# Kernel optimization log

Measured on AMD Instinct MI355X. Metric: run time of the kernel, lower is better.

Reference implementation:

```python
import jax, jax.numpy as jnp
import numpy as np

D_MODEL = 1024
N_HEAD = 16
D_HEAD = D_MODEL // N_HEAD
NEG = -1e9


def setup_inputs() -> dict:
    key = jax.random.key(0)
    ks = jax.random.split(key, 11)
    B, T, C = 4, 2048, D_MODEL
    s = 1.0 / np.sqrt(C)
    return {
        "q": jax.random.normal(ks[0], (B, T, C), jnp.float32),
        "k": jax.random.normal(ks[1], (B, T, C), jnp.float32),
        "v": jax.random.normal(ks[2], (B, T, C), jnp.float32),
        "w_q": jax.random.normal(ks[3], (C, C), jnp.float32) * s,
        "b_q": jnp.zeros((C,), jnp.float32),
        "w_k": jax.random.normal(ks[4], (C, C), jnp.float32) * s,
        "b_k": jnp.zeros((C,), jnp.float32),
        "w_v": jax.random.normal(ks[5], (C, C), jnp.float32) * s,
        "b_v": jnp.zeros((C,), jnp.float32),
        "w_o": jax.random.normal(ks[6], (C, C), jnp.float32) * s,
        "b_o": jnp.zeros((C,), jnp.float32),
    }


def reference(q, k, v, w_q, b_q, w_k, b_k, w_v, b_v, w_o, b_o):
    B, T, C = q.shape
    # projections; weights stored as [in, out]
    qh = (q @ w_q + b_q).reshape(B, T, N_HEAD, D_HEAD).transpose(0, 2, 1, 3)
    kh = (k @ w_k + b_k).reshape(B, T, N_HEAD, D_HEAD).transpose(0, 2, 1, 3)
    vh = (v @ w_v + b_v).reshape(B, T, N_HEAD, D_HEAD).transpose(0, 2, 1, 3)
    scores = jnp.einsum("bhqd,bhkd->bhqk", qh, kh) / jnp.sqrt(
        jnp.asarray(D_HEAD, qh.dtype))
    causal = jnp.tril(jnp.ones((T, T), dtype=bool))  # [T,T]
    scores = jnp.where(causal[None, None], scores, NEG)
    attn = jax.nn.softmax(scores, axis=-1)
    out = jnp.einsum("bhqk,bhkd->bhqd", attn, vh)
    out = out.transpose(0, 2, 1, 3).reshape(B, T, C)
    return out @ w_o + b_o
```

## Files before the change

### kernel.cpp

```cpp
#include <hip/hip_runtime.h>
#include <hip/hip_bf16.h>
#include <cstdint>
#include <cstddef>

#define DEVI static __device__ __forceinline__

typedef __attribute__((ext_vector_type(8))) short short8;
typedef __attribute__((ext_vector_type(4))) float f32x4;

typedef __attribute__((address_space(1))) const unsigned int as1c_uint;
typedef __attribute__((address_space(3))) unsigned int as3_uint;

constexpr int Bn = 4, Tn = 2048, Cn = 1024, Hn = 16, Dn = 64;
constexpr int Mtot = Bn * Tn;
#define QSCALE (0.125f * 1.44269504088896340736f)

DEVI unsigned short f2bf(float f) {
  unsigned u = __float_as_uint(f);
  u += 0x7fffu + ((u >> 16) & 1u);
  return (unsigned short)(u >> 16);
}
DEVI unsigned short f2bf_t(float f) {
  return (unsigned short)(__float_as_uint(f) >> 16);
}

DEVI void async16(const void* g, void* l) {
  __builtin_amdgcn_global_load_lds((as1c_uint*)g, (as3_uint*)l, 16, 0, 0);
}

__global__ __launch_bounds__(256) void transpose_cvt4(
    const float* __restrict__ w0, const float* __restrict__ w1,
    const float* __restrict__ w2, const float* __restrict__ w3,
    unsigned short* __restrict__ o0, unsigned short* __restrict__ o1,
    unsigned short* __restrict__ o2, unsigned short* __restrict__ o3) {
  __shared__ float tile[32][33];
  const int z = blockIdx.z;
  const float* w = z == 0 ? w0 : z == 1 ? w1 : z == 2 ? w2 : w3;
  unsigned short* wT = z == 0 ? o0 : z == 1 ? o1 : z == 2 ? o2 : o3;
  int n0 = blockIdx.x * 32, k0 = blockIdx.y * 32;
  int tx = threadIdx.x, ty = threadIdx.y;
#pragma unroll
  for (int r = 0; r < 32; r += 8)
    tile[ty + r][tx] = w[(size_t)(k0 + ty + r) * Cn + n0 + tx];
  __syncthreads();
  const int t = ty * 32 + tx;
  const int n_l = t >> 3;
  const int kq = (t & 7) * 4;
  const int n = n0 + n_l, k = k0 + kq;
  ushort4 pk;
#pragma unroll
  for (int e = 0; e < 4; ++e) ((unsigned short*)&pk)[e] = f2bf(tile[kq + e][n_l]);
  size_t idx = (size_t)((((n >> 4) * 32 + (k >> 5)) * 64 + ((k >> 3) & 3) * 16 + (n & 15))) * 8 + (k & 7);
  *(ushort4*)&wT[idx] = pk;
}

DEVI short8 xfrag(const unsigned short* Xlds, int i, int kc, int l15, int l4) {
  int row = i * 16 + l15;
  return *(const short8*)&Xlds[row * 1024 + (((kc * 4 + l4) ^ (row & 7)) * 8)];
}

template <int IB, int NJ, bool SWAP>
DEVI void proj_core(const unsigned short* __restrict__ wF,
                    const unsigned short* Xlds, int njb, int lane,
                    f32x4 (&acc)[IB][NJ]) {
  const int l15 = lane & 15, l4 = lane >> 4;
  const short8* wp = (const short8*)wF;
  short8 wfA[NJ], wfB[NJ];
#pragma unroll
  for (int j = 0; j < NJ; ++j) wfA[j] = wp[(size_t)((njb + j) * 32) * 64 + lane];
#pragma unroll 1
  for (int kc = 0; kc < 32; kc += 2) {
#pragma unroll
    for (int j = 0; j < NJ; ++j)
      wfB[j] = wp[(size_t)((njb + j) * 32 + kc + 1) * 64 + lane];
    short8 xf[IB];
#pragma unroll
    for (int i = 0; i < IB; ++i) xf[i] = xfrag(Xlds, i, kc, l15, l4);
#pragma unroll
    for (int i = 0; i < IB; ++i)
#pragma unroll
      for (int j = 0; j < NJ; ++j)
        acc[i][j] = SWAP
            ? __builtin_amdgcn_mfma_f32_16x16x32_bf16(xf[i], wfA[j], acc[i][j], 0, 0, 0)
            : __builtin_amdgcn_mfma_f32_16x16x32_bf16(wfA[j], xf[i], acc[i][j], 0, 0, 0);
    if (kc + 2 < 32) {
#pragma unroll
      for (int j = 0; j < NJ; ++j)
        wfA[j] = wp[(size_t)((njb + j) * 32 + kc + 2) * 64 + lane];
    }
#pragma unroll
    for (int i = 0; i < IB; ++i) xf[i] = xfrag(Xlds, i, kc + 1, l15, l4);
#pragma unroll
    for (int i = 0; i < IB; ++i)
#pragma unroll
      for (int j = 0; j < NJ; ++j)
        acc[i][j] = SWAP
            ? __builtin_amdgcn_mfma_f32_16x16x32_bf16(xf[i], wfB[j], acc[i][j], 0, 0, 0)
            : __builtin_amdgcn_mfma_f32_16x16x32_bf16(wfB[j], xf[i], acc[i][j], 0, 0, 0);
  }
}

DEVI void stage64_f32(const float* __restrict__ src, int m0,
                      unsigned short* Xlds, int tid) {
#pragma unroll
  for (int it = 0; it < 8; ++it) {
    int g = it * 1024 + tid;
    int row = g >> 7, slot = g & 127;
    const float4* p = (const float4*)(src + (size_t)(m0 + row) * Cn + slot * 8);
    float4 a = p[0], b = p[1];
    short8 sv;
    sv[0] = (short)f2bf(a.x); sv[1] = (short)f2bf(a.y);
    sv[2] = (short)f2bf(a.z); sv[3] = (short)f2bf(a.w);
    sv[4] = (short)f2bf(b.x); sv[5] = (short)f2bf(b.y);
    sv[6] = (short)f2bf(b.z); sv[7] = (short)f2bf(b.w);
    *(short8*)&Xlds[row * 1024 + ((slot ^ (row & 7)) * 8)] = sv;
  }
}

DEVI void stage64_bf(const unsigned short* __restrict__ src, int m0,
                     unsigned short* Xlds, int tid) {
#pragma unroll
  for (int it = 0; it < 8; ++it) {
    int s = it * 1024 + tid;
    int row = s >> 7, sl = s & 127;
    async16(src + (size_t)(m0 + row) * Cn + ((sl ^ (row & 7)) * 8),
            Xlds + (size_t)(it * 1024 + (tid & ~63)) * 8);
  }
}

__global__ __launch_bounds__(1024, 4) void proj_qkv(
    const float* __restrict__ xqf, const float* __restrict__ xkf,
    const float* __restrict__ xvf, const unsigned short* __restrict__ wFq,
    const unsigned short* __restrict__ wFk, const unsigned short* __restrict__ wFv,
    const float* __restrict__ bq, const float* __restrict__ bk,
    const float* __restrict__ bv, unsigned short* __restrict__ oq,
    unsigned short* __restrict__ ok, unsigned short* __restrict__ ov) {
  __shared__ unsigned short Xlds[64 * 1024];
  const int tid = threadIdx.x, lane = tid & 63, w = tid >> 6;
  const int l15 = lane & 15, l4 = lane >> 4;
  const int bid = blockIdx.x;
  const int z = bid >> 8;
  const int r = bid & 255;
  const int m0 = (r >> 1) * 64;
  const int nh = r & 1;
  const float* xz = z == 0 ? xqf : z == 1 ? xkf : xvf;
  const unsigned short* wF = z == 0 ? wFq : z == 1 ? wFk : wFv;
  const float* bias = z == 0 ? bq : z == 1 ? bk : bv;

  stage64_f32(xz, m0, Xlds, tid);
  __syncthreads();

  const f32x4 zf = {0.f, 0.f, 0.f, 0.f};
  f32x4 acc[4][2];
#pragma unroll
  for (int i = 0; i < 4; ++i)
#pragma unroll
    for (int j = 0; j < 2; ++j) acc[i][j] = zf;

  const int njb = nh * 32 + w * 2;
  if (z < 2)
    proj_core<4, 2, false>(wF, Xlds, njb, lane, acc);
  else
    proj_core<4, 2, true>(wF, Xlds, njb, lane, acc);

  const int b = m0 >> 11, t0loc = m0 & 2047;
  if (z < 2) {
    unsigned short* o = z == 0 ? oq : ok;
    const float scale = z == 0 ? QSCALE : 1.f;
#pragma unroll
    for (int j = 0; j < 2; ++j) {
      int ng = njb + j;
      int h = ng >> 2, d0 = (ng & 3) * 16 + l4 * 4;
      float4 bv4 = *(const float4*)&bias[ng * 16 + l4 * 4];
#pragma unroll
      for (int i = 0; i < 4; ++i) {
        int t = t0loc + i * 16 + l15;
        ushort4 pk;
        pk.x = f2bf((acc[i][j][0] + bv4.x) * scale);
        pk.y = f2bf((acc[i][j][1] + bv4.y) * scale);
        pk.z = f2bf((acc[i][j][2] + bv4.z) * scale);
        pk.w = f2bf((acc[i][j][3] + bv4.w) * scale);
        *(ushort4*)&o[((size_t)((b * Hn + h) * Tn + t)) * Dn + d0] = pk;
      }
    }
  } else {
#pragma unroll
    for (int j = 0; j < 2; ++j) {
      int n = (njb + j) * 16 + l15;
      int h = n >> 6, d = n & 63;
      float bvl = bias[n];
#pragma unroll
      for (int i = 0; i < 4; ++i) {
        int t0 = t0loc + i * 16 + l4 * 4;
        ushort4 pk;
        pk.x = f2bf(acc[i][j][0] + bvl);
        pk.y = f2bf(acc[i][j][1] + bvl);
        pk.z = f2bf(acc[i][j][2] + bvl);
        pk.w = f2bf(acc[i][j][3] + bvl);
        *(ushort4*)&ov[((size_t)((b * Hn + h) * Dn + d)) * Tn + t0] = pk;
      }
    }
  }
}

__global__ __launch_bounds__(1024, 4) void proj_out(
    const unsigned short* __restrict__ A, const unsigned short* __restrict__ wFo,
    const float* __restrict__ bias, float* __restrict__ o) {
  __shared__ unsigned short Xlds[64 * 1024];
  const int tid = threadIdx.x, lane = tid & 63, w = tid >> 6;
  const int l15 = lane & 15, l4 = lane >> 4;
  const int bid = blockIdx.x;
  const int m0 = (bid >> 1) * 64, nh = bid & 1;

  stage64_bf(A, m0, Xlds, tid);
  __syncthreads();

  const f32x4 zf = {0.f, 0.f, 0.f, 0.f};
  f32x4 acc[4][2];
#pragma unroll
  for (int i = 0; i < 4; ++i)
#pragma unroll
    for (int j = 0; j < 2; ++j) acc[i][j] = zf;

  const int njb = nh * 32 + w * 2;
  proj_core<4, 2, false>(wFo, Xlds, njb, lane, acc);

#pragma unroll
  for (int j = 0; j < 2; ++j) {
    int ng = njb + j;
    float4 bv4 = *(const float4*)&bias[ng * 16 + l4 * 4];
#pragma unroll
    for (int i = 0; i < 4; ++i) {
      int m = m0 + i * 16 + l15;
      float4 ov4;
      ov4.x = acc[i][j][0] + bv4.x;
      ov4.y = acc[i][j][1] + bv4.y;
      ov4.z = acc[i][j][2] + bv4.z;
      ov4.w = acc[i][j][3] + bv4.w;
      *(float4*)&o[(size_t)m * Cn + ng * 16 + l4 * 4] = ov4;
    }
  }
}

__global__ __launch_bounds__(512) void attn_kernel(const unsigned short* __restrict__ qh,
                                                   const unsigned short* __restrict__ kh,
                                                   const unsigned short* __restrict__ vt,
                                                   unsigned short* __restrict__ obf) {
  __shared__ unsigned short Ks[2][64 * 64];
  __shared__ unsigned short Vs[2][64 * 64];
  __shared__ unsigned short Ps[8][16 * 72];

  const int tid = threadIdx.x, lane = tid & 63, w = tid >> 6;
  const int l15 = lane & 15, l4 = lane >> 4;
  const int swz = l15 & 7;

  const int bid = blockIdx.x;
  const int j = bid >> 3;
  const int bh = (bid & 7) * 8 + (j & 7);
  const int pair = j >> 3;
  const unsigned short* qb = qh + (size_t)bh * Tn * Dn;
  const unsigned short* kb = kh + (size_t)bh * Tn * Dn;
  const unsigned short* vb = vt + (size_t)bh * Dn * Tn;
  const int b = bh >> 4, h = bh & 15;

  const int srow = lane >> 3, sslot = (lane & 7) ^ (lane >> 3);

  const f32x4 z = {0.f, 0.f, 0.f, 0.f};
  const short ob = (short)0x3F80;
  const short8 ones = {ob, ob, ob, ob, ob, ob, ob, ob};

#pragma unroll 1
  for (int half = 0; half < 2; ++half) {
    const int qt = half == 0 ? pair : 15 - pair;
    const int q0 = qt * 128;
    const int qrow = q0 + w * 16 + l15;

    short8 qf0 = *(const short8*)(qb + (size_t)qrow * Dn + l4 * 8);
    short8 qf1 = *(const short8*)(qb + (size_t)qrow * Dn + 32 + l4 * 8);

    f32x4 o[4];
#pragma unroll
    for (int nd = 0; nd < 4; ++nd) o[nd] = z;
    f32x4 osum = z;

    const int nt = (q0 >> 6) + 2;
    const int ntw = ((q0 + w * 16 + 15) >> 6) + 1;

    {
      const unsigned short* ksrc = kb + (size_t)(w * 8 + srow) * Dn + sslot * 8;
      const unsigned short* vsrc = vb + (size_t)(w * 8 + srow) * Tn + sslot * 8;
      async16(ksrc, &Ks[0][w * 512]);
      async16(vsrc, &Vs[0][w * 512]);
    }

#pragma unroll 1
    for (int t = 0; t < nt; ++t) {
      const int cur = t & 1;
      if (t + 1 < nt) {
        const int kv1 = (t + 1) * 64;
        const unsigned short* ksrc = kb + (size_t)(kv1 + w * 8 + srow) * Dn + sslot * 8;
        const unsigned short* vsrc = vb + (size_t)(w * 8 + srow) * Tn + kv1 + sslot * 8;
        async16(ksrc, &Ks[cur ^ 1][w * 512]);
        async16(vsrc, &Vs[cur ^ 1][w * 512]);
        asm volatile("s_waitcnt vmcnt(2)" ::: "memory");
      } else {
        asm volatile("s_waitcnt vmcnt(0)" ::: "memory");
      }
      __builtin_amdgcn_s_barrier();
      __builtin_amdgcn_sched_barrier(0);

      if (t < ntw) {
        const unsigned short* Kc = &Ks[cur][0];
        const unsigned short* Vc = &Vs[cur][0];

        f32x4 s[4];
#pragma unroll
        for (int ni = 0; ni < 4; ++ni) s[ni] = z;
        __builtin_amdgcn_s_setprio(1);
#pragma unroll
        for (int ni = 0; ni < 4; ++ni) {
          const int rb = (ni * 16 + l15) * 64;
          short8 kf0 = *(const short8*)&Kc[rb + ((l4 ^ swz) * 8)];
          short8 kf1 = *(const short8*)&Kc[rb + (((4 + l4) ^ swz) * 8)];
          s[ni] = __builtin_amdgcn_mfma_f32_16x16x32_bf16(kf0, qf0, s[ni], 0, 0, 0);
          s[ni] = __builtin_amdgcn_mfma_f32_16x16x32_bf16(kf1, qf1, s[ni], 0, 0, 0);
        }
        __builtin_amdgcn_s_setprio(0);

        short8 vf[8];
#pragma unroll
        for (int nd = 0; nd < 4; ++nd) {
          const int rb = (nd * 16 + l15) * 64;
          vf[nd * 2]     = *(const short8*)&Vc[rb + ((l4 ^ swz) * 8)];
          vf[nd * 2 + 1] = *(const short8*)&Vc[rb + (((4 + l4) ^ swz) * 8)];
        }

        const int kq = qrow - t * 64;
        const bool edge = (t * 64 + 63 > q0 + w * 16);
        if (!edge) {
#pragma unroll
          for (int ni = 0; ni < 4; ++ni) {
            ushort4 pk;
#pragma unroll
            for (int r = 0; r < 4; ++r)
              ((unsigned short*)&pk)[r] = f2bf_t(__builtin_amdgcn_exp2f(s[ni][r]));
            *(ushort4*)&Ps[w][l15 * 72 + ni * 16 + l4 * 4] = pk;
          }
        } else {
#pragma unroll
          for (int ni = 0; ni < 4; ++ni) {
            ushort4 pk;
#pragma unroll
            for (int r = 0; r < 4; ++r) {
              float e = __builtin_amdgcn_exp2f(s[ni][r]);
              if ((ni * 16 + l4 * 4 + r) > kq) e = 0.f;
              ((unsigned short*)&pk)[r] = f2bf_t(e);
            }
            *(ushort4*)&Ps[w][l15 * 72 + ni * 16 + l4 * 4] = pk;
          }
        }
        asm volatile("s_waitcnt lgkmcnt(0)" ::: "memory");
        __builtin_amdgcn_sched_barrier(0);

        short8 pf0 = *(const short8*)&Ps[w][l15 * 72 + l4 * 8];
        short8 pf1 = *(const short8*)&Ps[w][l15 * 72 + 32 + l4 * 8];
        __builtin_amdgcn_s_setprio(1);
        osum = __builtin_amdgcn_mfma_f32_16x16x32_bf16(pf0, ones, osum, 0, 0, 0);
        osum = __builtin_amdgcn_mfma_f32_16x16x32_bf16(pf1, ones, osum, 0, 0, 0);
#pragma unroll
        for (int nd = 0; nd < 4; ++nd) {
          o[nd] = __builtin_amdgcn_mfma_f32_16x16x32_bf16(pf0, vf[nd * 2], o[nd], 0, 0, 0);
          o[nd] = __builtin_amdgcn_mfma_f32_16x16x32_bf16(pf1, vf[nd * 2 + 1], o[nd], 0, 0, 0);
        }
        __builtin_amdgcn_s_setprio(0);
      }

      __builtin_amdgcn_sched_barrier(0);
      __builtin_amdgcn_s_barrier();
    }

#pragma unroll
    for (int r = 0; r < 4; ++r) {
      float inv = __builtin_amdgcn_rcpf(osum[r]);
      int tq = q0 + w * 16 + l4 * 4 + r;
      size_t base = ((size_t)(b * Tn + tq)) * Cn + h * 64;
#pragma unroll
      for (int nd = 0; nd < 4; ++nd)
        obf[base + nd * 16 + l15] = f2bf(o[nd][r] * inv);
    }
  }
}

extern "C" void kernel_launch(void* const* d_in, const int* in_sizes, int n_in,
                              void* d_out, int out_size, void* d_ws, size_t ws_size,
                              hipStream_t stream) {
  const float* q   = (const float*)d_in[0];
  const float* k   = (const float*)d_in[1];
  const float* v   = (const float*)d_in[2];
  const float* w_q = (const float*)d_in[3];
  const float* b_q = (const float*)d_in[4];
  const float* w_k = (const float*)d_in[5];
  const float* b_k = (const float*)d_in[6];
  const float* w_v = (const float*)d_in[7];
  const float* b_v = (const float*)d_in[8];
  const float* w_o = (const float*)d_in[9];
  const float* b_o = (const float*)d_in[10];

  char* ws = (char*)d_ws;
  const size_t MB = 1u << 20;
  unsigned short* qhp  = (unsigned short*)(ws);
  unsigned short* khp  = (unsigned short*)(ws + 16 * MB);
  unsigned short* vtp  = (unsigned short*)(ws + 32 * MB);
  unsigned short* aout = (unsigned short*)(ws + 48 * MB);
  unsigned short* wqT  = (unsigned short*)(ws + 64 * MB);
  unsigned short* wkT  = (unsigned short*)(ws + 66 * MB);
  unsigned short* wvT  = (unsigned short*)(ws + 68 * MB);
  unsigned short* woT  = (unsigned short*)(ws + 70 * MB);

  transpose_cvt4<<<dim3(32, 32, 4), dim3(32, 8), 0, stream>>>(
      w_q, w_k, w_v, w_o, wqT, wkT, wvT, woT);

  proj_qkv<<<768, 1024, 0, stream>>>(q, k, v, wqT, wkT, wvT,
                                     b_q, b_k, b_v, qhp, khp, vtp);

  attn_kernel<<<512, 512, 0, stream>>>(qhp, khp, vtp, aout);

  proj_out<<<256, 1024, 0, stream>>>(aout, woT, b_o, (float*)d_out);
}
```

Before: 169.1 us.

## Process q/k/v projections in one persistent block with prefetched input staging

The QKV projection kernel now launches 256 blocks that each loop over the three projections, instead of 768 blocks that each handle one. The next input tile's fp32 global loads are issued into registers before the current MFMA loop runs, so load latency overlaps compute. The cost is 64 extra VGPRs per thread for the staging buffer, with the launch-bounds occupancy hint dropped. There are also only 256 blocks for 256 CUs, one block per CU, which cuts the parallelism available to hide latency.

```diff
diff --git a/kernel.cpp b/kernel.cpp
--- a/kernel.cpp
+++ b/kernel.cpp
@@ -100,14 +100,24 @@
   }
 }
 
-DEVI void stage64_f32(const float* __restrict__ src, int m0,
-                      unsigned short* Xlds, int tid) {
+DEVI void stage_issue(const float* __restrict__ src, int m0, int tid,
+                      float4 (&st)[16]) {
 #pragma unroll
   for (int it = 0; it < 8; ++it) {
     int g = it * 1024 + tid;
     int row = g >> 7, slot = g & 127;
     const float4* p = (const float4*)(src + (size_t)(m0 + row) * Cn + slot * 8);
-    float4 a = p[0], b = p[1];
+    st[it * 2] = p[0];
+    st[it * 2 + 1] = p[1];
+  }
+}
+
+DEVI void stage_write(const float4 (&st)[16], unsigned short* Xlds, int tid) {
+#pragma unroll
+  for (int it = 0; it < 8; ++it) {
+    int g = it * 1024 + tid;
+    int row = g >> 7, slot = g & 127;
+    float4 a = st[it * 2], b = st[it * 2 + 1];
     short8 sv;
     sv[0] = (short)f2bf(a.x); sv[1] = (short)f2bf(a.y);
     sv[2] = (short)f2bf(a.z); sv[3] = (short)f2bf(a.w);
@@ -128,7 +138,7 @@
   }
 }
 
-__global__ __launch_bounds__(1024, 4) void proj_qkv(
+__global__ __launch_bounds__(1024) void proj_qkv(
     const float* __restrict__ xqf, const float* __restrict__ xkf,
     const float* __restrict__ xvf, const unsigned short* __restrict__ wFq,
     const unsigned short* __restrict__ wFk, const unsigned short* __restrict__ wFv,
@@ -139,65 +149,78 @@
   const int tid = threadIdx.x, lane = tid & 63, w = tid >> 6;
   const int l15 = lane & 15, l4 = lane >> 4;
   const int bid = blockIdx.x;
-  const int z = bid >> 8;
-  const int r = bid & 255;
-  const int m0 = (r >> 1) * 64;
-  const int nh = r & 1;
-  const float* xz = z == 0 ? xqf : z == 1 ? xkf : xvf;
-  const unsigned short* wF = z == 0 ? wFq : z == 1 ? wFk : wFv;
-  const float* bias = z == 0 ? bq : z == 1 ? bk : bv;
-
-  stage64_f32(xz, m0, Xlds, tid);
-  __syncthreads();
-
-  const f32x4 zf = {0.f, 0.f, 0.f, 0.f};
-  f32x4 acc[4][2];
-#pragma unroll
-  for (int i = 0; i < 4; ++i)
-#pragma unroll
-    for (int j = 0; j < 2; ++j) acc[i][j] = zf;
-
+  const int m0 = (bid >> 1) * 64;
+  const int nh = bid & 1;
   const int njb = nh * 32 + w * 2;
-  if (z < 2)
-    proj_core<4, 2, false>(wF, Xlds, njb, lane, acc);
-  else
-    proj_core<4, 2, true>(wF, Xlds, njb, lane, acc);
-
   const int b = m0 >> 11, t0loc = m0 & 2047;
-  if (z < 2) {
-    unsigned short* o = z == 0 ? oq : ok;
-    const float scale = z == 0 ? QSCALE : 1.f;
-#pragma unroll
-    for (int j = 0; j < 2; ++j) {
-      int ng = njb + j;
-      int h = ng >> 2, d0 = (ng & 3) * 16 + l4 * 4;
-      float4 bv4 = *(const float4*)&bias[ng * 16 + l4 * 4];
-#pragma unroll
-      for (int i = 0; i < 4; ++i) {
-        int t = t0loc + i * 16 + l15;
-        ushort4 pk;
-        pk.x = f2bf((acc[i][j][0] + bv4.x) * scale);
-        pk.y = f2bf((acc[i][j][1] + bv4.y) * scale);
-        pk.z = f2bf((acc[i][j][2] + bv4.z) * scale);
-        pk.w = f2bf((acc[i][j][3] + bv4.w) * scale);
-        *(ushort4*)&o[((size_t)((b * Hn + h) * Tn + t)) * Dn + d0] = pk;
+
+  float4 st[16];
+  stage_issue(xqf, m0, tid, st);
+  __builtin_amdgcn_sched_barrier(0);
+
+#pragma unroll 1
+  for (int z = 0; z < 3; ++z) {
+    asm volatile("s_waitcnt vmcnt(0)" ::: "memory");
+    stage_write(st, Xlds, tid);
+    __syncthreads();
+
+    if (z < 2) {
+      stage_issue(z == 0 ? xkf : xvf, m0, tid, st);
+      __builtin_amdgcn_sched_barrier(0);
+    }
+
+    const unsigned short* wF = z == 0 ? wFq : z == 1 ? wFk : wFv;
+    const float* bias = z == 0 ? bq : z == 1 ? bk : bv;
+
+    const f32x4 zf = {0.f, 0.f, 0.f, 0.f};
+    f32x4 acc[4][2];
+#pragma unroll
+    for (int i = 0; i < 4; ++i)
+#pragma unroll
+      for (int j = 0; j < 2; ++j) acc[i][j] = zf;
+
+    if (z < 2)
+      proj_core<4, 2, false>(wF, Xlds, njb, lane, acc);
+    else
+      proj_core<4, 2, true>(wF, Xlds, njb, lane, acc);
+
+    __syncthreads();
+
+    if (z < 2) {
+      unsigned short* o = z == 0 ? oq : ok;
+      const float scale = z == 0 ? QSCALE : 1.f;
+#pragma unroll
+      for (int j = 0; j < 2; ++j) {
+        int ng = njb + j;
+        int h = ng >> 2, d0 = (ng & 3) * 16 + l4 * 4;
+        float4 bv4 = *(const float4*)&bias[ng * 16 + l4 * 4];
+#pragma unroll
+        for (int i = 0; i < 4; ++i) {
+          int t = t0loc + i * 16 + l15;
+          ushort4 pk;
+          pk.x = f2bf((acc[i][j][0] + bv4.x) * scale);
+          pk.y = f2bf((acc[i][j][1] + bv4.y) * scale);
+          pk.z = f2bf((acc[i][j][2] + bv4.z) * scale);
+          pk.w = f2bf((acc[i][j][3] + bv4.w) * scale);
+          *(ushort4*)&o[((size_t)((b * Hn + h) * Tn + t)) * Dn + d0] = pk;
+        }
       }
-    }
-  } else {
-#pragma unroll
-    for (int j = 0; j < 2; ++j) {
-      int n = (njb + j) * 16 + l15;
-      int h = n >> 6, d = n & 63;
-      float bvl = bias[n];
-#pragma unroll
-      for (int i = 0; i < 4; ++i) {
-        int t0 = t0loc + i * 16 + l4 * 4;
-        ushort4 pk;
-        pk.x = f2bf(acc[i][j][0] + bvl);
-        pk.y = f2bf(acc[i][j][1] + bvl);
-        pk.z = f2bf(acc[i][j][2] + bvl);
-        pk.w = f2bf(acc[i][j][3] + bvl);
-        *(ushort4*)&ov[((size_t)((b * Hn + h) * Dn + d)) * Tn + t0] = pk;
+    } else {
+#pragma unroll
+      for (int j = 0; j < 2; ++j) {
+        int n = (njb + j) * 16 + l15;
+        int h = n >> 6, d = n & 63;
+        float bvl = bias[n];
+#pragma unroll
+        for (int i = 0; i < 4; ++i) {
+          int t0 = t0loc + i * 16 + l4 * 4;
+          ushort4 pk;
+          pk.x = f2bf(acc[i][j][0] + bvl);
+          pk.y = f2bf(acc[i][j][1] + bvl);
+          pk.z = f2bf(acc[i][j][2] + bvl);
+          pk.w = f2bf(acc[i][j][3] + bvl);
+          *(ushort4*)&ov[((size_t)((b * Hn + h) * Dn + d)) * Tn + t0] = pk;
+        }
       }
     }
   }
@@ -420,7 +443,7 @@
   transpose_cvt4<<<dim3(32, 32, 4), dim3(32, 8), 0, stream>>>(
       w_q, w_k, w_v, w_o, wqT, wkT, wvT, woT);
 
-  proj_qkv<<<768, 1024, 0, stream>>>(q, k, v, wqT, wkT, wvT,
+  proj_qkv<<<256, 1024, 0, stream>>>(q, k, v, wqT, wkT, wvT,
                                      b_q, b_k, b_v, qhp, khp, vtp);
 
   attn_kernel<<<512, 512, 0, stream>>>(qhp, khp, vtp, aout);
```

Result: slower. 199.0 us (+17.7%).
